# Performance work log

Measured on AMD Instinct MI355X. Metric: run time of the kernel, lower is better.

Reference implementation:

```python
import jax, jax.numpy as jnp
import numpy as np

N = 32768  # number of leaf states (rows); power of 2 for a clean Fenwick tree
D = 256    # embed_dim


def tree_cell(W, b, hl, cl, hr, cr):
    """Binary TreeLSTM cell: gates from [h_l; h_r], per-child forget gates."""
    z = jnp.concatenate([hl, hr], axis=-1) @ W + b  # [*, 5D]
    i, o, u, fl, fr = jnp.split(z, 5, axis=-1)
    c = jax.nn.sigmoid(i) * jnp.tanh(u) + jax.nn.sigmoid(fl) * cl + jax.nn.sigmoid(fr) * cr
    h = jax.nn.sigmoid(o) * jnp.tanh(c)
    return h, c


def setup_inputs() -> dict:
    key = jax.random.key(0)
    ks = jax.random.split(key, 6)
    s = 0.05  # glorot-ish scale for 512-fan-in weights
    return {
        "h_bot": jax.random.normal(ks[0], (N, D), jnp.float32),
        "c_bot": jax.random.normal(ks[1], (N, D), jnp.float32),
        "W_merge": jax.random.normal(ks[2], (2 * D, 5 * D), jnp.float32) * s,
        "b_merge": jnp.zeros((5 * D,), jnp.float32),
        "W_sum": jax.random.normal(ks[3], (2 * D, 5 * D), jnp.float32) * s,
        "b_sum": jnp.zeros((5 * D,), jnp.float32),
    }


def _fenwick(h_bot, c_bot, W_merge, b_merge, W_sum, b_sum):
    L = N.bit_length() - 1  # 15 tree levels above the leaves
    # --- build Fenwick tree: level k node j covers leaves [j*2^k, (j+1)*2^k) ---
    levels_h, levels_c = [h_bot], [c_bot]
    for k in range(1, L + 1):
        ph, pc = levels_h[-1], levels_c[-1]
        h, c = tree_cell(W_merge, b_merge, ph[0::2], pc[0::2], ph[1::2], pc[1::2])
        levels_h.append(h)
        levels_c.append(c)
    # --- per-prefix summary: for each t in 1..N fold the set-bit nodes of t ---
    # (matches FenwickTree.forward: levels ascending, state = summary(state, node))
    t = jnp.arange(1, N + 1)
    state_h = jnp.zeros((N, D), h_bot.dtype)
    state_c = jnp.zeros((N, D), h_bot.dtype)
    valid = jnp.zeros((N,), bool)
    for k in range(L + 1):
        has = (((t >> k) & 1) == 1)
        # node covering the trailing 2^k block of prefix t at level k
        idx = jnp.clip((t >> (k + 1)) * 2, 0, levels_h[k].shape[0] - 1)
        node_h = levels_h[k][idx]  # irregular gather  [N, D]
        node_c = levels_c[k][idx]
        nh, nc = tree_cell(W_sum, b_sum, state_h, state_c, node_h, node_c)
        m, v = has[:, None], valid[:, None]
        state_h = jnp.where(m, jnp.where(v, nh, node_h), state_h)
        state_c = jnp.where(m, jnp.where(v, nc, node_c), state_c)
        valid = valid | has
    return jnp.concatenate([state_h, state_c], axis=-1)  # [N, 2D]: (row_h, row_c)


def reference(h_bot, c_bot, W_merge, b_merge, W_sum, b_sum):
    return _fenwick(h_bot, c_bot, W_merge, b_merge, W_sum, b_sum)
```

## Files before the change

### kernel.cpp

```cpp
#include <hip/hip_runtime.h>
#include <hip/hip_bf16.h>


typedef unsigned short u16;
typedef unsigned int u32;
using short8  = __attribute__((ext_vector_type(8))) short;
using float4v = __attribute__((ext_vector_type(4))) float;


__device__ __forceinline__ u16 f2bf(float f) {
  u32 u = __float_as_uint(f);
  u = (u + 0x7FFFu + ((u >> 16) & 1u)) >> 16;
  return (u16)u;
}
__device__ __forceinline__ float bf2f(u16 h) {
  return __uint_as_float(((u32)h) << 16);
}
__device__ __forceinline__ float sigf(float x) { return 1.0f / (1.0f + __expf(-x)); }
__device__ __forceinline__ float tanhfast(float x) {
  return 2.0f / (1.0f + __expf(-2.0f * x)) - 1.0f;
}

__device__ __forceinline__ void async16(const void* g, void* l) {
  __builtin_amdgcn_global_load_lds((const __attribute__((address_space(1))) void*)g,
                                   (__attribute__((address_space(3))) void*)l,
                                   16, 0, 0);
}

__device__ __forceinline__ void row_srcs(int mode, int k, int row,
                                         const u16* h0b, const u16* hlv, const u16* sth,
                                         const u16*& pL, const u16*& pR) {
  if (mode == 0) {
    const u16* pb = (k == 1) ? h0b : (hlv + (size_t)(32768 - (1 << (17 - k))) * 256);
    pL = pb + (size_t)(2 * row) * 256;
    pR = pb + (size_t)(2 * row + 1) * 256;
  } else {
    const int Dk = (1 << k) - 1;
    const int i = row + row / Dk + 1;
    const int t = ((i >> k) << (k + 1)) | (1 << k) | (i & Dk);
    pL = sth + (size_t)(t - 1) * 256;
    const int idx = (t >> (k + 1)) * 2;
    pR = hlv + (size_t)((32768 - (1 << (16 - k))) + idx) * 256;
  }
}

__global__ __launch_bounds__(256) void gemm_cell(
    int mode, int k, int Mc,
    const u16* WT, const float* bias,
    const u16* h0b, const u16* hlv, const u16* sth_in,
    const float* cpar, float* cout, u16* hout,
    const float* clv, float* out, u16* sth_out)
{
  __shared__ __align__(16) u16 smem[18432];
  const int tid  = threadIdx.x;
  const int lane = tid & 63;
  const int w    = tid >> 6;
  const int wm   = w >> 1, wn = w & 1;

  const int nwg = gridDim.x;
  const int q8  = nwg >> 3;
  const int id  = (blockIdx.x & 7) * q8 + (blockIdx.x >> 3);
  const int bm  = id >> 3, bn = id & 7;

  const int f0 = w * 128 + lane;
  const int f1 = f0 + 64;
  int rl0 = bm * 128 + (f0 >> 2); if (rl0 > Mc - 1) rl0 = Mc - 1;
  int rl1 = bm * 128 + (f1 >> 2); if (rl1 > Mc - 1) rl1 = Mc - 1;
  const u16 *p0L, *p0R, *p1L, *p1R;
  row_srcs(mode, k, rl0, h0b, hlv, sth_in, p0L, p0R);
  row_srcs(mode, k, rl1, h0b, hlv, sth_in, p1L, p1R);
  const int sa0 = (f0 & 3) * 8, sa1 = (f1 & 3) * 8;
  u16* ldsA0 = smem + (w * 2 + 0) * 512;
  u16* ldsA1 = smem + (w * 2 + 1) * 512;

  const int ch0 = 0 * 4 + w, ch1 = 1 * 4 + w, ch2 = 2 * 4 + w;
  const u16* pB0 = WT + (size_t)(bn * 160 + ch0 * 16 + (lane >> 2)) * 512 + (lane & 3) * 8;
  const u16* pB1 = WT + (size_t)(bn * 160 + ch1 * 16 + (lane >> 2)) * 512 + (lane & 3) * 8;
  const u16* pB2 = (ch2 < 10)
      ? WT + (size_t)(bn * 160 + ch2 * 16 + (lane >> 2)) * 512 + (lane & 3) * 8
      : pB0;
  u16* ldsB0 = smem + 4096 + ch0 * 512;
  u16* ldsB1 = smem + 4096 + ch1 * 512;
  u16* ldsB2 = smem + 4096 + (ch2 < 10 ? ch2 : 0) * 512;

  float4v acc[4][5];
#pragma unroll
  for (int i = 0; i < 4; ++i)
#pragma unroll
    for (int j = 0; j < 5; ++j) acc[i][j] = (float4v){0.f, 0.f, 0.f, 0.f};

  const int mrow = lane & 15;
  const int kg   = lane >> 4;
  const u16* aBase = smem + (wm * 64 + mrow) * 32 + kg * 8;
  const u16* bBase = smem + 4096 + (wn * 16 + mrow) * 32 + kg * 8;

  auto stage = [&](int bo, int kk) {
    const u16* s0 = (kk < 8) ? (p0L + sa0 + kk * 32) : (p0R + sa0 + (kk - 8) * 32);
    const u16* s1 = (kk < 8) ? (p1L + sa1 + kk * 32) : (p1R + sa1 + (kk - 8) * 32);
    async16(s0, ldsA0 + bo);
    async16(s1, ldsA1 + bo);
    async16(pB0 + kk * 32, ldsB0 + bo);
    async16(pB1 + kk * 32, ldsB1 + bo);
    if (ch2 < 10) async16(pB2 + kk * 32, ldsB2 + bo);
  };

  stage(0, 0);
  asm volatile("s_waitcnt vmcnt(0)" ::: "memory");
  __builtin_amdgcn_s_barrier();

#pragma unroll 2
  for (int kk = 0; kk < 16; ++kk) {
    const int cu = (kk & 1) * 9216;
    if (kk < 15) stage(9216 - cu, kk + 1);
    short8 af[4], bfv[5];
    const u16* aB = aBase + cu;
    const u16* bB = bBase + cu;
#pragma unroll
    for (int mt = 0; mt < 4; ++mt) af[mt]  = *(const short8*)(aB + mt * 512);
#pragma unroll
    for (int g = 0; g < 5; ++g)   bfv[g]  = *(const short8*)(bB + g * 1024);
#pragma unroll
    for (int mt = 0; mt < 4; ++mt)
#pragma unroll
      for (int g = 0; g < 5; ++g)
        acc[mt][g] = __builtin_amdgcn_mfma_f32_16x16x32_bf16(af[mt], bfv[g], acc[mt][g], 0, 0, 0);
    asm volatile("s_waitcnt vmcnt(0)" ::: "memory");
    __builtin_amdgcn_s_barrier();
  }

  const int d = bn * 32 + wn * 16 + mrow;
  const float bi  = bias[d];
  const float bo_ = bias[256 + d];
  const float bu  = bias[512 + d];
  const float bfl = bias[768 + d];
  const float bfr2= bias[1024 + d];

#pragma unroll
  for (int mt = 0; mt < 4; ++mt) {
    const int r0 = bm * 128 + wm * 64 + mt * 16 + kg * 4;
#pragma unroll
    for (int r = 0; r < 4; ++r) {
      const int row = r0 + r;
      if (row >= Mc) continue;
      const float zi  = acc[mt][0][r] + bi;
      const float zo  = acc[mt][1][r] + bo_;
      const float zu  = acc[mt][2][r] + bu;
      const float zfl = acc[mt][3][r] + bfl;
      const float zfr = acc[mt][4][r] + bfr2;
      if (mode == 0) {
        const float cl = cpar[(size_t)(2 * row) * 256 + d];
        const float cr = cpar[(size_t)(2 * row + 1) * 256 + d];
        const float c = sigf(zi) * tanhfast(zu) + sigf(zfl) * cl + sigf(zfr) * cr;
        const float h = sigf(zo) * tanhfast(c);
        cout[(size_t)row * 256 + d] = c;
        hout[(size_t)row * 256 + d] = f2bf(h);
      } else {
        const int Dk  = (1 << k) - 1;
        const int i   = row + row / Dk + 1;
        const int t   = ((i >> k) << (k + 1)) | (1 << k) | (i & Dk);
        const int lk  = 32768 - (1 << (16 - k));
        const int idx = (t >> (k + 1)) * 2;
        const float cr = clv[(size_t)(lk + idx) * 256 + d];
        const float cl = out[(size_t)(t - 1) * 512 + 256 + d];
        const float c = sigf(zi) * tanhfast(zu) + sigf(zfl) * cl + sigf(zfr) * cr;
        const float h = sigf(zo) * tanhfast(c);
        out[(size_t)(t - 1) * 512 + 256 + d] = c;
        if ((i >> k) == 0) {
          out[(size_t)(t - 1) * 512 + d] = h;
        } else {
          sth_out[(size_t)(t - 1) * 256 + d] = f2bf(h);
        }
      }
    }
  }
}

__global__ __launch_bounds__(256) void merge_sth(
    int k, const u16* src, u16* dst)
{
  const int idx = blockIdx.x * 256 + threadIdx.x;
  const int i = idx >> 5;
  const int s = (idx & 31) * 8;
  const int mask = (1 << k) - 1;
  if ((i & mask) == 0 || (i >> k) == 0) return;
  const int t = ((i >> k) << (k + 1)) | (1 << k) | (i & mask);
  *(short8*)(dst + (size_t)(t - 1) * 256 + s) = *(const short8*)(src + (size_t)(t - 1) * 256 + s);
}

__global__ __launch_bounds__(256) void copy_k0(
    const float* __restrict__ h_bot, const float* __restrict__ c_bot,
    float* __restrict__ out, u16* __restrict__ sth)
{
  const int i = blockIdx.x;
  const int d = threadIdx.x;
  const int t = 2 * i + 1;
  const float h = h_bot[(size_t)(t - 1) * 256 + d];
  const float c = c_bot[(size_t)(t - 1) * 256 + d];
  if (i == 0) out[(size_t)(t - 1) * 512 + d] = h;
  out[(size_t)(t - 1) * 512 + 256 + d] = c;
  sth[(size_t)(t - 1) * 256 + d] = f2bf(h);
}

__global__ __launch_bounds__(256) void seed_even(
    const u16* __restrict__ hlv, const float* __restrict__ clv,
    float* __restrict__ out, u16* __restrict__ sth)
{
  const int j = blockIdx.x;
  const int t = 2 * j + 2;
  const int d = threadIdx.x;
  const int k = __ffs(t) - 1;
  const int lk = 32768 - (1 << (16 - k));
  const int nidx = (t >> (k + 1)) * 2;
  const u16 hb  = hlv[(size_t)(lk + nidx) * 256 + d];
  const float c = clv[(size_t)(lk + nidx) * 256 + d];
  out[(size_t)(t - 1) * 512 + 256 + d] = c;
  if ((t & (t - 1)) == 0) {
    out[(size_t)(t - 1) * 512 + d] = bf2f(hb);
  } else {
    sth[(size_t)(t - 1) * 256 + d] = hb;
  }
}

__global__ __launch_bounds__(256) void transpose_w(
    const float* __restrict__ W, u16* __restrict__ WT)
{
  const int n = blockIdx.x;
  const int b = n / 160, r = n % 160;
  const int g = r / 32,  dl = r % 32;
  const int col = g * 256 + b * 32 + dl;
  const int tid = threadIdx.x;
  WT[(size_t)n * 512 + tid]       = f2bf(W[(size_t)tid * 1280 + col]);
  WT[(size_t)n * 512 + tid + 256] = f2bf(W[(size_t)(tid + 256) * 1280 + col]);
}

__global__ __launch_bounds__(256) void cast_h0(
    const float* __restrict__ h, u16* __restrict__ h0b)
{
  const size_t i = (size_t)blockIdx.x * 256 + threadIdx.x;
  h0b[i] = f2bf(h[i]);
}

extern "C" void kernel_launch(void* const* d_in, const int* in_sizes, int n_in,
                              void* d_out, int out_size, void* d_ws, size_t ws_size,
                              hipStream_t stream) {
  const float* h_bot = (const float*)d_in[0];
  const float* c_bot = (const float*)d_in[1];
  const float* Wm    = (const float*)d_in[2];
  const float* bmv   = (const float*)d_in[3];
  const float* Wsu   = (const float*)d_in[4];
  const float* bsv   = (const float*)d_in[5];
  float* out = (float*)d_out;
  char* ws = (char*)d_ws;

  u16*   WmT  = (u16*)(ws + 0);
  u16*   WsT  = (u16*)(ws + 1310720);
  u16*   h0b  = (u16*)(ws + 2621440);
  u16*   hlv  = (u16*)(ws + 19398656);
  float* clv  = (float*)(ws + 36175872);
  u16*   sth  = (u16*)(ws + 69730304);
  u16*   sthN = (u16*)(ws + 86507520);

  transpose_w<<<1280, 256, 0, stream>>>(Wm, WmT);
  transpose_w<<<1280, 256, 0, stream>>>(Wsu, WsT);
  cast_h0<<<32768, 256, 0, stream>>>(h_bot, h0b);

  for (int kl = 1; kl <= 15; ++kl) {
    const int M = 32768 >> kl;
    const float* cpar = (kl == 1) ? c_bot : (clv + (size_t)(32768 - (1 << (17 - kl))) * 256);
    float* cout = clv + (size_t)(32768 - (1 << (16 - kl))) * 256;
    u16*   hout = hlv + (size_t)(32768 - (1 << (16 - kl))) * 256;
    const int nbm = (M + 127) / 128;
    gemm_cell<<<nbm * 8, 256, 0, stream>>>(0, kl, M, WmT, bmv, h0b, hlv, sth,
                                           cpar, cout, hout, clv, out, sthN);
  }

  copy_k0<<<16384, 256, 0, stream>>>(h_bot, c_bot, out, sth);
  seed_even<<<16384, 256, 0, stream>>>(hlv, clv, out, sth);
  for (int kl = 1; kl <= 14; ++kl) {
    const int M = 16384 - (16384 >> kl);
    const int nbm = (M + 127) / 128;
    gemm_cell<<<nbm * 8, 256, 0, stream>>>(1, kl, M, WsT, bsv, h0b, hlv, sth,
                                           nullptr, nullptr, nullptr, clv, out, sthN);
    if (kl <= 13) merge_sth<<<2048, 256, 0, stream>>>(kl, sthN, sth);
  }
}
```

Before: 1.153 ms.

## Ping-pong state buffers by popcount parity and widen GEMM K-tile with swizzled LDS

Replaces the separate merge_sth copy kernel with two state buffers chosen by the parity of popcount(i & mask), so each level reads from one buffer and writes into the other without a copy pass. The GEMM mainloop now stages 64-wide K slices (8 stages instead of 16), which doubles LDS use. It applies an XOR swizzle on the LDS layout to avoid bank conflicts and raises wave priority around the MFMA bursts. This is meant to cut kernel launches, copy traffic and barrier count, at the cost of more LDS per block, which may lower occupancy, and parity logic that must stay correct.

```diff
diff --git a/kernel.cpp b/kernel.cpp
--- a/kernel.cpp
+++ b/kernel.cpp
@@ -28,7 +28,8 @@
 }
 
 __device__ __forceinline__ void row_srcs(int mode, int k, int row,
-                                         const u16* h0b, const u16* hlv, const u16* sth,
+                                         const u16* h0b, const u16* hlv,
+                                         const u16* sthA, const u16* sthB,
                                          const u16*& pL, const u16*& pR) {
   if (mode == 0) {
     const u16* pb = (k == 1) ? h0b : (hlv + (size_t)(32768 - (1 << (17 - k))) * 256);
@@ -38,7 +39,9 @@
     const int Dk = (1 << k) - 1;
     const int i = row + row / Dk + 1;
     const int t = ((i >> k) << (k + 1)) | (1 << k) | (i & Dk);
-    pL = sth + (size_t)(t - 1) * 256;
+    const int c = __popc(i & Dk);
+    const u16* sb = (c & 1) ? sthB : sthA;
+    pL = sb + (size_t)(t - 1) * 256;
     const int idx = (t >> (k + 1)) * 2;
     pR = hlv + (size_t)((32768 - (1 << (16 - k))) + idx) * 256;
   }
@@ -47,11 +50,11 @@
 __global__ __launch_bounds__(256) void gemm_cell(
     int mode, int k, int Mc,
     const u16* WT, const float* bias,
-    const u16* h0b, const u16* hlv, const u16* sth_in,
+    const u16* h0b, const u16* hlv, u16* sthA, u16* sthB,
     const float* cpar, float* cout, u16* hout,
-    const float* clv, float* out, u16* sth_out)
-{
-  __shared__ __align__(16) u16 smem[18432];
+    const float* clv, float* out)
+{
+  __shared__ __align__(16) u16 smem[36864];
   const int tid  = threadIdx.x;
   const int lane = tid & 63;
   const int w    = tid >> 6;
@@ -62,26 +65,24 @@
   const int id  = (blockIdx.x & 7) * q8 + (blockIdx.x >> 3);
   const int bm  = id >> 3, bn = id & 7;
 
-  const int f0 = w * 128 + lane;
-  const int f1 = f0 + 64;
-  int rl0 = bm * 128 + (f0 >> 2); if (rl0 > Mc - 1) rl0 = Mc - 1;
-  int rl1 = bm * 128 + (f1 >> 2); if (rl1 > Mc - 1) rl1 = Mc - 1;
-  const u16 *p0L, *p0R, *p1L, *p1R;
-  row_srcs(mode, k, rl0, h0b, hlv, sth_in, p0L, p0R);
-  row_srcs(mode, k, rl1, h0b, hlv, sth_in, p1L, p1R);
-  const int sa0 = (f0 & 3) * 8, sa1 = (f1 & 3) * 8;
-  u16* ldsA0 = smem + (w * 2 + 0) * 512;
-  u16* ldsA1 = smem + (w * 2 + 1) * 512;
-
-  const int ch0 = 0 * 4 + w, ch1 = 1 * 4 + w, ch2 = 2 * 4 + w;
-  const u16* pB0 = WT + (size_t)(bn * 160 + ch0 * 16 + (lane >> 2)) * 512 + (lane & 3) * 8;
-  const u16* pB1 = WT + (size_t)(bn * 160 + ch1 * 16 + (lane >> 2)) * 512 + (lane & 3) * 8;
-  const u16* pB2 = (ch2 < 10)
-      ? WT + (size_t)(bn * 160 + ch2 * 16 + (lane >> 2)) * 512 + (lane & 3) * 8
-      : pB0;
-  u16* ldsB0 = smem + 4096 + ch0 * 512;
-  u16* ldsB1 = smem + 4096 + ch1 * 512;
-  u16* ldsB2 = smem + 4096 + (ch2 < 10 ? ch2 : 0) * 512;
+  const int rr  = lane >> 3;
+  const int seg = lane & 7;
+  const int swz = ((seg ^ rr) - seg) * 8;
+
+  const u16 *aL[4], *aR[4];
+#pragma unroll
+  for (int j = 0; j < 4; ++j) {
+    int rl = bm * 128 + (w * 4 + j) * 8 + rr;
+    if (rl > Mc - 1) rl = Mc - 1;
+    const u16 *pL, *pR;
+    row_srcs(mode, k, rl, h0b, hlv, sthA, sthB, pL, pR);
+    aL[j] = pL + seg * 8 + swz;
+    aR[j] = pR + seg * 8 + swz;
+  }
+  const u16* pB[5];
+#pragma unroll
+  for (int j = 0; j < 5; ++j)
+    pB[j] = WT + (size_t)(bn * 160 + (w * 5 + j) * 8 + rr) * 512 + seg * 8 + swz;
 
   float4v acc[4][5];
 #pragma unroll
@@ -91,42 +92,51 @@
 
   const int mrow = lane & 15;
   const int kg   = lane >> 4;
-  const u16* aBase = smem + (wm * 64 + mrow) * 32 + kg * 8;
-  const u16* bBase = smem + 4096 + (wn * 16 + mrow) * 32 + kg * 8;
-
-  auto stage = [&](int bo, int kk) {
-    const u16* s0 = (kk < 8) ? (p0L + sa0 + kk * 32) : (p0R + sa0 + (kk - 8) * 32);
-    const u16* s1 = (kk < 8) ? (p1L + sa1 + kk * 32) : (p1R + sa1 + (kk - 8) * 32);
-    async16(s0, ldsA0 + bo);
-    async16(s1, ldsA1 + bo);
-    async16(pB0 + kk * 32, ldsB0 + bo);
-    async16(pB1 + kk * 32, ldsB1 + bo);
-    if (ch2 < 10) async16(pB2 + kk * 32, ldsB2 + bo);
-  };
-
-  stage(0, 0);
-  asm volatile("s_waitcnt vmcnt(0)" ::: "memory");
-  __builtin_amdgcn_s_barrier();
-
-#pragma unroll 2
-  for (int kk = 0; kk < 16; ++kk) {
-    const int cu = (kk & 1) * 9216;
-    if (kk < 15) stage(9216 - cu, kk + 1);
-    short8 af[4], bfv[5];
-    const u16* aB = aBase + cu;
-    const u16* bB = bBase + cu;
-#pragma unroll
-    for (int mt = 0; mt < 4; ++mt) af[mt]  = *(const short8*)(aB + mt * 512);
-#pragma unroll
-    for (int g = 0; g < 5; ++g)   bfv[g]  = *(const short8*)(bB + g * 1024);
-#pragma unroll
-    for (int mt = 0; mt < 4; ++mt)
+  const int m7   = mrow & 7;
+
+#define STAGE(buf, kk2)                                                        \
+  {                                                                            \
+    const int offA = (kk2 & 3) * 64;                                           \
+    _Pragma("unroll")                                                          \
+    for (int j = 0; j < 4; ++j)                                                \
+      async16(((kk2) < 4 ? aL[j] : aR[j]) + offA,                              \
+              smem + (buf) * 8192 + (w * 4 + j) * 512);                        \
+    _Pragma("unroll")                                                          \
+    for (int j = 0; j < 5; ++j)                                                \
+      async16(pB[j] + (kk2) * 64,                                              \
+              smem + 16384 + (buf) * 10240 + (w * 5 + j) * 512);               \
+  }
+
+  STAGE(0, 0);
+  __syncthreads();
+
+#pragma unroll
+  for (int s = 0; s < 8; ++s) {
+    const int cur = s & 1;
+    if (s < 7) STAGE(cur ^ 1, s + 1);
+    const u16* aT = smem + cur * 8192;
+    const u16* bT = smem + 16384 + cur * 10240;
+#pragma unroll
+    for (int kkk = 0; kkk < 2; ++kkk) {
+      short8 af[4], bfv[5];
+      const int js = ((kkk * 4 + kg) ^ m7) * 8;
+#pragma unroll
+      for (int mt = 0; mt < 4; ++mt)
+        af[mt] = *(const short8*)(aT + (wm * 64 + mt * 16 + mrow) * 64 + js);
 #pragma unroll
       for (int g = 0; g < 5; ++g)
-        acc[mt][g] = __builtin_amdgcn_mfma_f32_16x16x32_bf16(af[mt], bfv[g], acc[mt][g], 0, 0, 0);
-    asm volatile("s_waitcnt vmcnt(0)" ::: "memory");
-    __builtin_amdgcn_s_barrier();
-  }
+        bfv[g] = *(const short8*)(bT + (g * 32 + wn * 16 + mrow) * 64 + js);
+      __builtin_amdgcn_s_setprio(1);
+#pragma unroll
+      for (int mt = 0; mt < 4; ++mt)
+#pragma unroll
+        for (int g = 0; g < 5; ++g)
+          acc[mt][g] = __builtin_amdgcn_mfma_f32_16x16x32_bf16(af[mt], bfv[g], acc[mt][g], 0, 0, 0);
+      __builtin_amdgcn_s_setprio(0);
+    }
+    __syncthreads();
+  }
+#undef STAGE
 
   const int d = bn * 32 + wn * 16 + mrow;
   const float bi  = bias[d];
@@ -168,28 +178,18 @@
         if ((i >> k) == 0) {
           out[(size_t)(t - 1) * 512 + d] = h;
         } else {
-          sth_out[(size_t)(t - 1) * 256 + d] = f2bf(h);
+          const int cpc = __popc(i & Dk);
+          u16* dst = (cpc & 1) ? sthA : sthB;
+          dst[(size_t)(t - 1) * 256 + d] = f2bf(h);
         }
       }
     }
   }
 }
 
-__global__ __launch_bounds__(256) void merge_sth(
-    int k, const u16* src, u16* dst)
-{
-  const int idx = blockIdx.x * 256 + threadIdx.x;
-  const int i = idx >> 5;
-  const int s = (idx & 31) * 8;
-  const int mask = (1 << k) - 1;
-  if ((i & mask) == 0 || (i >> k) == 0) return;
-  const int t = ((i >> k) << (k + 1)) | (1 << k) | (i & mask);
-  *(short8*)(dst + (size_t)(t - 1) * 256 + s) = *(const short8*)(src + (size_t)(t - 1) * 256 + s);
-}
-
 __global__ __launch_bounds__(256) void copy_k0(
     const float* __restrict__ h_bot, const float* __restrict__ c_bot,
-    float* __restrict__ out, u16* __restrict__ sth)
+    float* __restrict__ out, u16* __restrict__ sthB)
 {
   const int i = blockIdx.x;
   const int d = threadIdx.x;
@@ -198,12 +198,12 @@
   const float c = c_bot[(size_t)(t - 1) * 256 + d];
   if (i == 0) out[(size_t)(t - 1) * 512 + d] = h;
   out[(size_t)(t - 1) * 512 + 256 + d] = c;
-  sth[(size_t)(t - 1) * 256 + d] = f2bf(h);
+  sthB[(size_t)(t - 1) * 256 + d] = f2bf(h);
 }
 
 __global__ __launch_bounds__(256) void seed_even(
     const u16* __restrict__ hlv, const float* __restrict__ clv,
-    float* __restrict__ out, u16* __restrict__ sth)
+    float* __restrict__ out, u16* __restrict__ sthB)
 {
   const int j = blockIdx.x;
   const int t = 2 * j + 2;
@@ -217,7 +217,7 @@
   if ((t & (t - 1)) == 0) {
     out[(size_t)(t - 1) * 512 + d] = bf2f(hb);
   } else {
-    sth[(size_t)(t - 1) * 256 + d] = hb;
+    sthB[(size_t)(t - 1) * 256 + d] = hb;
   }
 }
 
@@ -257,8 +257,8 @@
   u16*   h0b  = (u16*)(ws + 2621440);
   u16*   hlv  = (u16*)(ws + 19398656);
   float* clv  = (float*)(ws + 36175872);
-  u16*   sth  = (u16*)(ws + 69730304);
-  u16*   sthN = (u16*)(ws + 86507520);
+  u16*   sthA = (u16*)(ws + 69730304);
+  u16*   sthB = (u16*)(ws + 86507520);
 
   transpose_w<<<1280, 256, 0, stream>>>(Wm, WmT);
   transpose_w<<<1280, 256, 0, stream>>>(Wsu, WsT);
@@ -270,17 +270,18 @@
     float* cout = clv + (size_t)(32768 - (1 << (16 - kl))) * 256;
     u16*   hout = hlv + (size_t)(32768 - (1 << (16 - kl))) * 256;
     const int nbm = (M + 127) / 128;
-    gemm_cell<<<nbm * 8, 256, 0, stream>>>(0, kl, M, WmT, bmv, h0b, hlv, sth,
-                                           cpar, cout, hout, clv, out, sthN);
-  }
-
-  copy_k0<<<16384, 256, 0, stream>>>(h_bot, c_bot, out, sth);
-  seed_even<<<16384, 256, 0, stream>>>(hlv, clv, out, sth);
+    gemm_cell<<<nbm * 8, 256, 0, stream>>>(0, kl, M, WmT, bmv, h0b, hlv,
+                                           sthA, sthB,
+                                           cpar, cout, hout, clv, out);
+  }
+
+  copy_k0<<<16384, 256, 0, stream>>>(h_bot, c_bot, out, sthB);
+  seed_even<<<16384, 256, 0, stream>>>(hlv, clv, out, sthB);
   for (int kl = 1; kl <= 14; ++kl) {
     const int M = 16384 - (16384 >> kl);
     const int nbm = (M + 127) / 128;
-    gemm_cell<<<nbm * 8, 256, 0, stream>>>(1, kl, M, WsT, bsv, h0b, hlv, sth,
-                                           nullptr, nullptr, nullptr, clv, out, sthN);
-    if (kl <= 13) merge_sth<<<2048, 256, 0, stream>>>(kl, sthN, sth);
-  }
-}
+    gemm_cell<<<nbm * 8, 256, 0, stream>>>(1, kl, M, WsT, bsv, h0b, hlv,
+                                           sthA, sthB,
+                                           nullptr, nullptr, nullptr, clv, out);
+  }
+}
```

Result: faster. 984.2 us (-14.7%).
